# Kernel optimization log

Measured on AMD Instinct MI355X. Metric: run time of the kernel, lower is better.

## Reference

```python
import jax, jax.numpy as jnp
import numpy as np


def setup_inputs() -> dict:
    key = jax.random.key(0)
    k1, k2 = jax.random.split(key)
    x = jax.random.normal(k1, (8, 512, 32, 14, 14), dtype=jnp.float32)
    # Conv1d(in=1, out=1, kernel=5, bias=False) weight, torch layout (O, I, K)
    conv_w = jax.random.normal(k2, (1, 1, 5), dtype=jnp.float32) * 0.2
    return {"x": x, "conv_w": conv_w}


def reference(x, conv_w):
    # x: (N, C, T, H, W)
    N, C, T = x.shape[:3]
    PAD = 2  # k=5, padding=k//2
    # Global average pool over H, W -> (N, C, T)
    gap = x.mean(axis=(3, 4))
    # Original loops over T applying Conv1d over the channel axis per timestep.
    # Batched equivalent: fold T into the batch dim -> (N*T, 1, C)
    seq = gap.transpose(0, 2, 1).reshape(N * T, 1, C)
    y = jax.lax.conv_general_dilated(
        seq, conv_w, window_strides=(1,), padding=[(PAD, PAD)],
        dimension_numbers=("NCH", "OIH", "NCH"))  # (N*T, 1, C)
    att = jax.nn.sigmoid(y.reshape(N, T, C).transpose(0, 2, 1))  # (N, C, T)
    return att[..., None, None]  # (N, C, T, 1, 1)
```

## Files before the change

### kernel.cpp

```cpp
#include <hip/hip_runtime.h>
#include <hip/hip_bf16.h>


#define F4_PER_ROW 49
#define CH 32
#define TBLK 2
#define HALO 2
#define ROWS_TOT ((CH + 2 * HALO) * TBLK)

__global__ __launch_bounds__(256, 8) void fused_halo_kernel(
        const float* __restrict__ x,
        const float* __restrict__ w,
        float* __restrict__ out) {
    const int bid = blockIdx.x;
    const int n   = bid >> 8;
    const int cb  = (bid >> 4) & 15;
    const int tb  = bid & 15;
    const int c0  = cb * CH;
    const int t0  = tb * TBLK;

    const int tid = threadIdx.x;
    const int q   = tid & 3;

    __shared__ float gs[ROWS_TOT];

    #pragma unroll
    for (int pass = 0; pass < 2; ++pass) {
        const int ri = pass * 64 + (tid >> 2);
        if (ri < ROWS_TOT) {
            const int ci = ri >> 1;
            const int tj = ri & 1;
            const int c  = c0 - HALO + ci;
            float sum = 0.0f;
            if (c >= 0 && c < 512) {
                const int row = (n * 512 + c) * 32 + t0 + tj;
                const float4* p = reinterpret_cast<const float4*>(x) +
                                  (size_t)row * F4_PER_ROW + q;
                float4 a0 = p[0];
                float4 a1 = p[4];
                #pragma unroll
                for (int i = 2; i < 12; i += 2) {
                    float4 u = p[4 * i];
                    float4 v = p[4 * (i + 1)];
                    a0.x += u.x; a0.y += u.y; a0.z += u.z; a0.w += u.w;
                    a1.x += v.x; a1.y += v.y; a1.z += v.z; a1.w += v.w;
                }
                sum = ((a0.x + a1.x) + (a0.y + a1.y)) +
                      ((a0.z + a1.z) + (a0.w + a1.w));
                if (q == 0) {
                    float4 u = p[48];
                    sum += (u.x + u.y) + (u.z + u.w);
                }
            }
            sum += __shfl_xor(sum, 1, 64);
            sum += __shfl_xor(sum, 2, 64);
            if (q == 0) gs[ri] = sum * (1.0f / 196.0f);
        }
    }
    __syncthreads();

    if (tid < CH * TBLK) {
        const int ci = tid >> 1;
        const int tj = tid & 1;
        const float acc =
            w[0] * gs[(ci + 0) * TBLK + tj] +
            w[1] * gs[(ci + 1) * TBLK + tj] +
            w[2] * gs[(ci + 2) * TBLK + tj] +
            w[3] * gs[(ci + 3) * TBLK + tj] +
            w[4] * gs[(ci + 4) * TBLK + tj];
        out[(n * 512 + c0 + ci) * 32 + t0 + tj] = 1.0f / (1.0f + __expf(-acc));
    }
}

extern "C" void kernel_launch(void* const* d_in, const int* in_sizes, int n_in,
                              void* d_out, int out_size, void* d_ws, size_t ws_size,
                              hipStream_t stream) {
    const float* x = (const float*)d_in[0];
    const float* w = (const float*)d_in[1];
    float* out = (float*)d_out;

    fused_halo_kernel<<<2048, 256, 0, stream>>>(x, w, out);
}
```

Before: 22.91 us.

## Widen channel tile to 128 with one timestep per block to shrink halo reloads

Each block now owns 128 channels at a single timestep instead of 32 channels by 2 timesteps. The conv halo overhead drops from 4 extra rows per 32 channels to 4 per 128, which cuts redundant global reads. Each thread accumulates two rows at once with interleaved loads for more memory-level parallelism, and the grid halves to 1024 blocks with launch bounds lowered to 4. The risks are fewer blocks for latency hiding, higher register pressure, and a serial tail where only 16 threads load the extra halo rows.

```diff
diff --git a/kernel.cpp b/kernel.cpp
--- a/kernel.cpp
+++ b/kernel.cpp
@@ -3,72 +3,111 @@
 
 
 #define F4_PER_ROW 49
-#define CH 32
-#define TBLK 2
-#define HALO 2
-#define ROWS_TOT ((CH + 2 * HALO) * TBLK)
+#define OWN_CH 128
+#define ROWS_TOT (OWN_CH + 4)
 
-__global__ __launch_bounds__(256, 8) void fused_halo_kernel(
+__device__ __forceinline__ float row_base_sum_single(
+        const float* __restrict__ x, int n, int c, int t, int q, float4* tail) {
+    const int row = (n * 512 + c) * 32 + t;
+    const float4* p = reinterpret_cast<const float4*>(x) +
+                      (size_t)row * F4_PER_ROW + q;
+    float4 a0 = p[0];
+    float4 a1 = p[4];
+    #pragma unroll
+    for (int i = 2; i < 12; i += 2) {
+        float4 u = p[4 * i];
+        float4 v = p[4 * (i + 1)];
+        a0.x += u.x; a0.y += u.y; a0.z += u.z; a0.w += u.w;
+        a1.x += v.x; a1.y += v.y; a1.z += v.z; a1.w += v.w;
+    }
+    float s = ((a0.x + a1.x) + (a0.y + a1.y)) + ((a0.z + a1.z) + (a0.w + a1.w));
+    if (q == 0) {
+        float4 u = p[48];
+        s += (u.x + u.y) + (u.z + u.w);
+    }
+    (void)tail;
+    return s;
+}
+
+__global__ __launch_bounds__(256, 4) void fused_halo2_kernel(
         const float* __restrict__ x,
         const float* __restrict__ w,
         float* __restrict__ out) {
     const int bid = blockIdx.x;
-    const int n   = bid >> 8;
-    const int cb  = (bid >> 4) & 15;
-    const int tb  = bid & 15;
-    const int c0  = cb * CH;
-    const int t0  = tb * TBLK;
+    const int n   = bid >> 7;
+    const int cb  = (bid >> 5) & 3;
+    const int t0  = bid & 31;
+    const int c0  = cb * OWN_CH;
 
     const int tid = threadIdx.x;
+    const int k   = tid >> 2;
     const int q   = tid & 3;
 
     __shared__ float gs[ROWS_TOT];
 
+    const int cA = c0 - 2 + k;
+    const int cB = c0 - 2 + k + 64;
+    const bool vA = (cA >= 0) && (cA < 512);
+    const bool vB = (cB >= 0) && (cB < 512);
+    const int rowA = (n * 512 + (vA ? cA : 0)) * 32 + t0;
+    const int rowB = (n * 512 + (vB ? cB : 0)) * 32 + t0;
+    const float4* pA = reinterpret_cast<const float4*>(x) +
+                       (size_t)rowA * F4_PER_ROW + q;
+    const float4* pB = reinterpret_cast<const float4*>(x) +
+                       (size_t)rowB * F4_PER_ROW + q;
+
+    float4 a0 = pA[0];
+    float4 b0 = pB[0];
+    float4 a1 = pA[4];
+    float4 b1 = pB[4];
     #pragma unroll
-    for (int pass = 0; pass < 2; ++pass) {
-        const int ri = pass * 64 + (tid >> 2);
-        if (ri < ROWS_TOT) {
-            const int ci = ri >> 1;
-            const int tj = ri & 1;
-            const int c  = c0 - HALO + ci;
-            float sum = 0.0f;
-            if (c >= 0 && c < 512) {
-                const int row = (n * 512 + c) * 32 + t0 + tj;
-                const float4* p = reinterpret_cast<const float4*>(x) +
-                                  (size_t)row * F4_PER_ROW + q;
-                float4 a0 = p[0];
-                float4 a1 = p[4];
-                #pragma unroll
-                for (int i = 2; i < 12; i += 2) {
-                    float4 u = p[4 * i];
-                    float4 v = p[4 * (i + 1)];
-                    a0.x += u.x; a0.y += u.y; a0.z += u.z; a0.w += u.w;
-                    a1.x += v.x; a1.y += v.y; a1.z += v.z; a1.w += v.w;
-                }
-                sum = ((a0.x + a1.x) + (a0.y + a1.y)) +
-                      ((a0.z + a1.z) + (a0.w + a1.w));
-                if (q == 0) {
-                    float4 u = p[48];
-                    sum += (u.x + u.y) + (u.z + u.w);
-                }
-            }
-            sum += __shfl_xor(sum, 1, 64);
-            sum += __shfl_xor(sum, 2, 64);
-            if (q == 0) gs[ri] = sum * (1.0f / 196.0f);
-        }
+    for (int i = 2; i < 12; i += 2) {
+        float4 uA = pA[4 * i];
+        float4 uB = pB[4 * i];
+        float4 vA4 = pA[4 * (i + 1)];
+        float4 vB4 = pB[4 * (i + 1)];
+        a0.x += uA.x; a0.y += uA.y; a0.z += uA.z; a0.w += uA.w;
+        b0.x += uB.x; b0.y += uB.y; b0.z += uB.z; b0.w += uB.w;
+        a1.x += vA4.x; a1.y += vA4.y; a1.z += vA4.z; a1.w += vA4.w;
+        b1.x += vB4.x; b1.y += vB4.y; b1.z += vB4.z; b1.w += vB4.w;
+    }
+    float sA = ((a0.x + a1.x) + (a0.y + a1.y)) + ((a0.z + a1.z) + (a0.w + a1.w));
+    float sB = ((b0.x + b1.x) + (b0.y + b1.y)) + ((b0.z + b1.z) + (b0.w + b1.w));
+    if (q == 0) {
+        float4 uA = pA[48];
+        float4 uB = pB[48];
+        sA += (uA.x + uA.y) + (uA.z + uA.w);
+        sB += (uB.x + uB.y) + (uB.z + uB.w);
+    }
+    sA += __shfl_xor(sA, 1, 64);
+    sA += __shfl_xor(sA, 2, 64);
+    sB += __shfl_xor(sB, 1, 64);
+    sB += __shfl_xor(sB, 2, 64);
+    if (q == 0) {
+        gs[k]      = vA ? sA * (1.0f / 196.0f) : 0.0f;
+        gs[k + 64] = vB ? sB * (1.0f / 196.0f) : 0.0f;
+    }
+
+    if (k < 4) {
+        const int r  = 128 + k;
+        const int c  = c0 - 2 + r;
+        const bool v = (c >= 0) && (c < 512);
+        float s = 0.0f;
+        if (v) s = row_base_sum_single(x, n, c, t0, q, nullptr);
+        s += __shfl_xor(s, 1, 64);
+        s += __shfl_xor(s, 2, 64);
+        if (q == 0) gs[r] = v ? s * (1.0f / 196.0f) : 0.0f;
     }
     __syncthreads();
 
-    if (tid < CH * TBLK) {
-        const int ci = tid >> 1;
-        const int tj = tid & 1;
+    if (tid < OWN_CH) {
         const float acc =
-            w[0] * gs[(ci + 0) * TBLK + tj] +
-            w[1] * gs[(ci + 1) * TBLK + tj] +
-            w[2] * gs[(ci + 2) * TBLK + tj] +
-            w[3] * gs[(ci + 3) * TBLK + tj] +
-            w[4] * gs[(ci + 4) * TBLK + tj];
-        out[(n * 512 + c0 + ci) * 32 + t0 + tj] = 1.0f / (1.0f + __expf(-acc));
+            w[0] * gs[tid + 0] +
+            w[1] * gs[tid + 1] +
+            w[2] * gs[tid + 2] +
+            w[3] * gs[tid + 3] +
+            w[4] * gs[tid + 4];
+        out[(n * 512 + c0 + tid) * 32 + t0] = 1.0f / (1.0f + __expf(-acc));
     }
 }
 
@@ -79,5 +118,5 @@
     const float* w = (const float*)d_in[1];
     float* out = (float*)d_out;
 
-    fused_halo_kernel<<<2048, 256, 0, stream>>>(x, w, out);
+    fused_halo2_kernel<<<1024, 256, 0, stream>>>(x, w, out);
 }
```

After: 24.48 us. 6.9% more time.
